# Kernel tuning notes

Hardware: AMD Instinct MI355X
Metric: run time of the kernel (lower is better)

Reference implementation:

```python
import jax, jax.numpy as jnp
import numpy as np
from jax import lax

EPS = 0.1        # entropic regularization
MAX_ITER = 100   # Sinkhorn iteration budget
THRESH = 0.1     # early-stop threshold on err = mean_b sum_i |u - u_prev|
B, N, D = 16, 1024, 64


def setup_inputs() -> dict:
    key = jax.random.key(0)
    k1, k2 = jax.random.split(key)
    x = jax.random.normal(k1, (B, N, D), dtype=jnp.float32)
    y = jax.random.normal(k2, (B, N, D), dtype=jnp.float32)
    return {"x": x, "y": y}


def _lse(A):
    # Faithful to the original (unstabilized) lse: log(sum(exp(A)) + 1e-6)
    return jnp.log(jnp.exp(A).sum(-1) + 1e-6)


def _M(C, u, v):
    # (-C_ij + u_i + v_j) / eps
    return (-C + u[..., :, None] + v[..., None, :]) / EPS


def _cost_matrix(x, y):
    # (avoids materializing the [B, N, N, D] difference tensor; same math for p=2)
    x2 = (x * x).sum(-1)                         # [B, N]
    y2 = (y * y).sum(-1)                         # [B, N]
    xy = jnp.einsum('bid,bjd->bij', x, y)        # [B, N, N]
    return x2[..., :, None] + y2[..., None, :] - 2.0 * xy


def reference(x, y):
    x = jax.nn.softmax(x, axis=-1)
    y = jax.nn.softmax(y, axis=-1)
    C = _cost_matrix(x, y)                       # [B, N, N]
    n = x.shape[-2]
    log_mu = jnp.log(1.0 / n + 1e-8)             # mu = nu = uniform 1/n (scalar broadcast)
    u0 = jnp.zeros((x.shape[0], n), dtype=C.dtype)
    v0 = jnp.zeros_like(u0)

    def cond(carry):
        _, _, i, err = carry
        return jnp.logical_and(i < MAX_ITER, err >= THRESH)

    def body(carry):
        u, v, i, _ = carry
        u1 = u
        u = EPS * (log_mu - _lse(_M(C, u, v))) + u
        v = EPS * (log_mu - _lse(jnp.swapaxes(_M(C, u, v), -2, -1))) + v
        err = jnp.abs(u - u1).sum(-1).mean()
        return (u, v, i + 1, err)

    u, v, _, _ = lax.while_loop(
        cond, body, (u0, v0, jnp.int32(0), jnp.float32(jnp.inf)))

    pi = jnp.exp(_M(C, u, v))                    # transport plan [B, N, N]
    cost = (pi * C).sum((-2, -1))                # [B]
    return cost.mean()                           # reduction='mean'
```

## Files before the change

kernel.cpp:

```cpp
#include <hip/hip_runtime.h>
#include <hip/hip_bf16.h>
#include <math.h>

#define BATCH 16
#define NPTS 1024
#define DIM 64
#define EPSF 0.1f
#define INV_EPS 10.0f
#define MAX_ITER 100
#define THRESHF 0.1f
#define LSTRIDE 72

typedef _Float16 h8 __attribute__((ext_vector_type(8)));
typedef short short8v __attribute__((ext_vector_type(8)));
typedef float float4v __attribute__((ext_vector_type(4)));

#define ATOMIC_ST(p, v) \
  __hip_atomic_store((p), (v), __ATOMIC_RELAXED, __HIP_MEMORY_SCOPE_AGENT)
#define ATOMIC_LD(p) \
  __hip_atomic_load((p), __ATOMIC_RELAXED, __HIP_MEMORY_SCOPE_AGENT)

__device__ inline float waveSum(float x) {
#pragma unroll
  for (int off = 32; off; off >>= 1) x += __shfl_xor(x, off, 64);
  return x;
}
__device__ inline float waveMax(float x) {
#pragma unroll
  for (int off = 32; off; off >>= 1) x = fmaxf(x, __shfl_xor(x, off, 64));
  return x;
}

__global__ __launch_bounds__(512, 1) void sinkhorn_fused(
    const float* __restrict__ x, const float* __restrict__ y,
    __hip_bfloat16* __restrict__ syh,
    float* __restrict__ y2,
    float* __restrict__ colsum,
    float* __restrict__ deltaPub,
    float* __restrict__ errB,
    int* __restrict__ flags,
    float* __restrict__ costPart,
    float* __restrict__ out) {
  __shared__ __attribute__((aligned(16))) short xs[64 * LSTRIDE];
  __shared__ __attribute__((aligned(16))) short ys[2][64 * LSTRIDE];
  __shared__ __attribute__((aligned(16))) short os[2][64 * LSTRIDE];
  __shared__ __attribute__((aligned(16))) float wLDS[NPTS];
  __shared__ __attribute__((aligned(16))) float vLDS[NPTS];
  __shared__ __attribute__((aligned(16))) float colpart[8][NPTS];
  __shared__ float x2L[64];
  __shared__ float derr[8];
  __shared__ float errbL[BATCH];
  const int t = threadIdx.x;
  const int blk = blockIdx.x;
  const int wave = t >> 6, lane = t & 63;
  const int batch = (blk & 7) + 8 * (blk >> 7);
  const int kslot = (blk >> 3) & 15;
  const float log_mu = logf(1.0f / 1024.0f + 1e-8f);

#pragma unroll
  for (int rr = 0; rr < 8; rr++) {
    int rl = wave * 8 + rr;
    int gr = batch * NPTS + kslot * 64 + rl;
    float xv = x[(size_t)gr * DIM + lane];
    float mx = waveMax(xv);
    float ex = expf(xv - mx);
    float sx = waveSum(ex);
    float px = ex / sx;
    __hip_bfloat16 hbx = (__hip_bfloat16)px;
    xs[rl * LSTRIDE + lane] = *(const short*)&hbx;
    float sqx = waveSum(px * px);
    if (lane == 0) x2L[rl] = sqx;
    float yv = y[(size_t)gr * DIM + lane];
    float my = waveMax(yv);
    float ey = expf(yv - my);
    float sy = waveSum(ey);
    float py = ey / sy;
    __hip_bfloat16 hby = (__hip_bfloat16)py;
    unsigned bits = *(const unsigned short*)&hby;
    unsigned nb = __shfl_down(bits, 1);
    if ((lane & 1) == 0)
      ATOMIC_ST((unsigned*)((unsigned short*)syh + (size_t)gr * DIM + lane),
                bits | (nb << 16));
    float sqy = waveSum(py * py);
    if (lane == 0) ATOMIC_ST(&y2[gr], sqy);
  }
  if (t < 192) {
    int buf = t >> 6, j = kslot * 64 + (t & 63);
    ATOMIC_ST(&colsum[((size_t)buf * BATCH + batch) * NPTS + j], 0.f);
  }
  __syncthreads();
  if (t == 0) ATOMIC_ST(&flags[batch * 16 + kslot], 1);
  if (t < 16) {
    while (ATOMIC_LD(&flags[batch * 16 + t]) < 1) {}
  }
  __syncthreads();

  const int m = lane & 15, q = lane >> 4;
  const int g = lane >> 3, sub = lane & 7;
  const int sw = wave & 3, ts = wave >> 2;
  short8v a0 = *(const short8v*)&xs[(sw * 16 + m) * LSTRIDE + q * 8];
  short8v a1 = *(const short8v*)&xs[(sw * 16 + m) * LSTRIDE + 32 + q * 8];
  float xa[4];
#pragma unroll
  for (int reg = 0; reg < 4; reg++) xa[reg] = x2L[sw * 16 + q * 4 + reg];
  h8 ka[8], kb[8];
#pragma unroll
  for (int k = 0; k < 8; k++) {
    {
      int idx = t;
#pragma unroll
      for (int rep = 0; rep < 2; rep++, idx += 512) {
        int r = idx >> 3, c = idx & 7;
        *(short8v*)&ys[r >> 6][(r & 63) * LSTRIDE + c * 8] = *(const short8v*)(
            (const short*)syh + ((size_t)batch * NPTS + 128 * k + r) * DIM + c * 8);
      }
    }
    __syncthreads();
    const int jt = 2 * k + ts;
    float4v accv[4];
#pragma unroll
    for (int tj = 0; tj < 4; tj++) {
      short8v b0 = *(const short8v*)&ys[ts][(tj * 16 + m) * LSTRIDE + q * 8];
      short8v b1 = *(const short8v*)&ys[ts][(tj * 16 + m) * LSTRIDE + 32 + q * 8];
      float4v c = {0.f, 0.f, 0.f, 0.f};
      c = __builtin_amdgcn_mfma_f32_16x16x32_bf16(a0, b0, c, 0, 0, 0);
      c = __builtin_amdgcn_mfma_f32_16x16x32_bf16(a1, b1, c, 0, 0, 0);
      accv[tj] = c;
    }
#pragma unroll
    for (int tj = 0; tj < 4; tj++) {
      float y2v = y2[(size_t)batch * NPTS + jt * 64 + tj * 16 + m];
#pragma unroll
      for (int reg = 0; reg < 4; reg++) {
        float C = xa[reg] + y2v - 2.0f * accv[tj][reg];
        _Float16 kv = (_Float16)expf(-INV_EPS * C);
        os[ts][(sw * 16 + q * 4 + reg) * LSTRIDE + tj * 16 + m] = *(const short*)&kv;
      }
    }
    __syncthreads();
    {
      int e0 = (2 * k) & 7, e1 = (2 * k + 1) & 7;
      if (g == e0 || g == e1) {
        const short* srcp = (g == e0) ? &os[0][0] : &os[1][0];
#pragma unroll
        for (int rr = 0; rr < 8; rr++) {
          h8 v = *(const h8*)&srcp[(wave * 8 + rr) * LSTRIDE + sub * 8];
          if (k < 4) ka[rr] = v; else kb[rr] = v;
        }
      }
    }
    __syncthreads();
  }

  for (int j = t; j < NPTS; j += 512) { vLDS[j] = 0.f; wLDS[j] = 1.f; }
  __syncthreads();

  float u[8], uPrev[8];
#pragma unroll
  for (int r = 0; r < 8; r++) u[r] = 0.f;
  int it = 0;

  while (true) {
#pragma unroll
    for (int r = 0; r < 8; r++) uPrev[r] = u[r];
    const float4* w4 = (const float4*)wLDS;
    float wreg[16];
    *(float4*)&wreg[0]  = w4[2 * lane];
    *(float4*)&wreg[4]  = w4[2 * lane + 1];
    *(float4*)&wreg[8]  = w4[128 + 2 * lane];
    *(float4*)&wreg[12] = w4[128 + 2 * lane + 1];
    float colreg[16];
#pragma unroll
    for (int n = 0; n < 16; n++) colreg[n] = 0.f;
    float delta = 0.f;
#pragma unroll
    for (int rr = 0; rr < 8; rr++) {
      float kf[16];
#pragma unroll
      for (int n = 0; n < 8; n++) {
        kf[n] = (float)ka[rr][n];
        kf[8 + n] = (float)kb[rr][n];
      }
      float dot = 0.f;
#pragma unroll
      for (int n = 0; n < 16; n++) dot = fmaf(kf[n], wreg[n], dot);
      dot = waveSum(dot);
      float uo = u[rr];
      float s = expf(INV_EPS * uo) * dot;
      float un = EPSF * (log_mu - logf(s + 1e-6f)) + uo;
      delta += fabsf(un - uo);
      u[rr] = un;
      float ai = expf(INV_EPS * un);
#pragma unroll
      for (int n = 0; n < 16; n++) colreg[n] = fmaf(kf[n], ai, colreg[n]);
    }
    if (lane == 0) derr[wave] = delta;
    {
      float4* cp = (float4*)&colpart[wave][0];
      cp[2 * lane]       = make_float4(colreg[0], colreg[1], colreg[2], colreg[3]);
      cp[2 * lane + 1]   = make_float4(colreg[4], colreg[5], colreg[6], colreg[7]);
      cp[128 + 2 * lane] = make_float4(colreg[8], colreg[9], colreg[10], colreg[11]);
      cp[128 + 2 * lane + 1] = make_float4(colreg[12], colreg[13], colreg[14], colreg[15]);
    }
    __syncthreads();
    float* cs = colsum + ((size_t)(it % 3) * BATCH + batch) * NPTS;
#pragma unroll
    for (int rep = 0; rep < 2; rep++) {
      int j = t + rep * 512;
      float s = 0.f;
#pragma unroll
      for (int w = 0; w < 8; w++) s += colpart[w][j];
      unsafeAtomicAdd(&cs[j], s);
    }
    if (t == 0) {
      float e = 0.f;
#pragma unroll
      for (int w = 0; w < 8; w++) e += derr[w];
      ATOMIC_ST(&deltaPub[((it & 1) * BATCH + batch) * 16 + kslot], e);
    }
    __syncthreads();
    if (t == 0) ATOMIC_ST(&flags[batch * 16 + kslot], it + 2);
    if (t < 16) {
      while (ATOMIC_LD(&flags[batch * 16 + t]) < it + 2) {}
    }
    __syncthreads();
    float cs0 = ATOMIC_LD(&cs[t]);
    float cs1 = ATOMIC_LD(&cs[t + 512]);
    if (t < 64)
      ATOMIC_ST(&colsum[((size_t)((it + 2) % 3) * BATCH + batch) * NPTS +
                        kslot * 64 + t], 0.f);
    if (kslot == 0 && t == 0) {
      const float* dp = deltaPub + ((it & 1) * BATCH + batch) * 16;
      float e = 0.f;
#pragma unroll
      for (int k = 0; k < 16; k++) e += ATOMIC_LD((float*)&dp[k]);
      ATOMIC_ST(&errB[it * BATCH + batch], e);
    }
    if (it >= 1) {
      if (t < BATCH) {
        float v;
        while ((v = ATOMIC_LD(&errB[(it - 1) * BATCH + t])) < 0.f) {}
        errbL[t] = v;
      }
      __syncthreads();
      float errv = 0.f;
#pragma unroll
      for (int k = 0; k < BATCH; k++) errv += errbL[k];
      if (errv * (1.0f / (float)BATCH) < THRESHF) {
#pragma unroll
        for (int r = 0; r < 8; r++) u[r] = uPrev[r];
        break;
      }
    }
    {
      float vo = vLDS[t];
      float s = expf(INV_EPS * vo) * cs0;
      float vn = EPSF * (log_mu - logf(s + 1e-6f)) + vo;
      vLDS[t] = vn;
      wLDS[t] = expf(INV_EPS * vn);
      float vo1 = vLDS[t + 512];
      float s1 = expf(INV_EPS * vo1) * cs1;
      float vn1 = EPSF * (log_mu - logf(s1 + 1e-6f)) + vo1;
      vLDS[t + 512] = vn1;
      wLDS[t + 512] = expf(INV_EPS * vn1);
    }
    it++;
    if (it >= MAX_ITER) break;
    __syncthreads();
  }

  {
    __syncthreads();
    const float4* w4 = (const float4*)wLDS;
    float wreg[16];
    *(float4*)&wreg[0]  = w4[2 * lane];
    *(float4*)&wreg[4]  = w4[2 * lane + 1];
    *(float4*)&wreg[8]  = w4[128 + 2 * lane];
    *(float4*)&wreg[12] = w4[128 + 2 * lane + 1];
    float csum = 0.f;
#pragma unroll
    for (int rr = 0; rr < 8; rr++) {
      float kf[16];
#pragma unroll
      for (int n = 0; n < 8; n++) {
        kf[n] = (float)ka[rr][n];
        kf[8 + n] = (float)kb[rr][n];
      }
      float ai = expf(INV_EPS * u[rr]);
#pragma unroll
      for (int n = 0; n < 16; n++) {
        if (kf[n] > 0.f)
          csum += ai * wreg[n] * kf[n] * (-EPSF * logf(kf[n]));
      }
    }
    csum = waveSum(csum);
    if (lane == 0) derr[wave] = csum;
    __syncthreads();
    if (t == 0) {
      float cst = 0.f;
#pragma unroll
      for (int w = 0; w < 8; w++) cst += derr[w];
      ATOMIC_ST(&costPart[blk], cst + 1.0f);
    }
    if (blk == 0) {
      if (t < 256) {
        float v;
        while ((v = ATOMIC_LD(&costPart[t])) < 0.5f) {}
        colpart[0][t] = v;
      }
      __syncthreads();
      if (wave == 0) {
        float s = colpart[0][lane] + colpart[0][lane + 64] +
                  colpart[0][lane + 128] + colpart[0][lane + 192];
        s = waveSum(s);
        if (lane == 0) out[0] = (s - 256.0f) * (1.0f / (float)BATCH);
      }
    }
  }
}

extern "C" void kernel_launch(void* const* d_in, const int* in_sizes, int n_in,
                              void* d_out, int out_size, void* d_ws,
                              size_t ws_size, hipStream_t stream) {
  (void)in_sizes; (void)n_in; (void)out_size; (void)ws_size;
  const float* x = (const float*)d_in[0];
  const float* y = (const float*)d_in[1];
  float* out = (float*)d_out;

  char* ws = (char*)d_ws;
  size_t off = 0;
  auto alloc = [&](size_t nbytes) -> void* {
    void* p = (void*)(ws + off);
    off = (off + nbytes + 255) & ~(size_t)255;
    return p;
  };
  __hip_bfloat16* syh = (__hip_bfloat16*)alloc((size_t)BATCH * NPTS * DIM * 2);
  float* y2 = (float*)alloc((size_t)BATCH * NPTS * 4);
  float* colsum = (float*)alloc((size_t)3 * BATCH * NPTS * 4);
  float* deltaPub = (float*)alloc((size_t)2 * BATCH * 16 * 4);
  float* errB = (float*)alloc((size_t)MAX_ITER * BATCH * 4);
  int* flags = (int*)alloc((size_t)BATCH * 16 * 4);
  float* costPart = (float*)alloc(256 * 4);

  void* args[] = {&x, &y, &syh, &y2, &colsum, &deltaPub,
                  &errB, &flags, &costPart, &out};
  hipLaunchCooperativeKernel((void*)sinkhorn_fused, dim3(256), dim3(512), args,
                             0, stream);
}
```

Before: 136.1 us.

## Assign two batches per block to overlap cross-block sync with other batch's work

```diff
diff --git a/kernel.cpp b/kernel.cpp
--- a/kernel.cpp
+++ b/kernel.cpp
@@ -10,6 +10,7 @@
 #define MAX_ITER 100
 #define THRESHF 0.1f
 #define LSTRIDE 72
+#define OSTRIDE 136
 
 typedef _Float16 h8 __attribute__((ext_vector_type(8)));
 typedef short short8v __attribute__((ext_vector_type(8)));
@@ -42,10 +43,11 @@
     float* __restrict__ costPart,
     float* __restrict__ out) {
   __shared__ __attribute__((aligned(16))) short xs[64 * LSTRIDE];
-  __shared__ __attribute__((aligned(16))) short ys[2][64 * LSTRIDE];
-  __shared__ __attribute__((aligned(16))) short os[2][64 * LSTRIDE];
-  __shared__ __attribute__((aligned(16))) float wLDS[NPTS];
-  __shared__ __attribute__((aligned(16))) float vLDS[NPTS];
+  __shared__ __attribute__((aligned(16))) short ysA[128 * LSTRIDE];
+  __shared__ __attribute__((aligned(16))) short ysB[128 * LSTRIDE];
+  __shared__ __attribute__((aligned(16))) short os[2][32 * OSTRIDE];
+  __shared__ __attribute__((aligned(16))) float wV[2][NPTS];
+  __shared__ __attribute__((aligned(16))) float vV[2][NPTS];
   __shared__ __attribute__((aligned(16))) float colpart[8][NPTS];
   __shared__ float x2L[64];
   __shared__ float derr[8];
@@ -53,23 +55,25 @@
   const int t = threadIdx.x;
   const int blk = blockIdx.x;
   const int wave = t >> 6, lane = t & 63;
-  const int batch = (blk & 7) + 8 * (blk >> 7);
-  const int kslot = (blk >> 3) & 15;
+  const int slot = blk >> 3;
+  const int batchA = (blk & 7) * 2;
+  const int batchB = batchA + 1;
   const float log_mu = logf(1.0f / 1024.0f + 1e-8f);
 
 #pragma unroll
   for (int rr = 0; rr < 8; rr++) {
-    int rl = wave * 8 + rr;
-    int gr = batch * NPTS + kslot * 64 + rl;
+    int idx = wave * 8 + rr;
+    int batch = (idx < 32) ? batchA : batchB;
+    int gr = batch * NPTS + slot * 32 + (idx & 31);
     float xv = x[(size_t)gr * DIM + lane];
     float mx = waveMax(xv);
     float ex = expf(xv - mx);
     float sx = waveSum(ex);
     float px = ex / sx;
     __hip_bfloat16 hbx = (__hip_bfloat16)px;
-    xs[rl * LSTRIDE + lane] = *(const short*)&hbx;
+    xs[idx * LSTRIDE + lane] = *(const short*)&hbx;
     float sqx = waveSum(px * px);
-    if (lane == 0) x2L[rl] = sqx;
+    if (lane == 0) x2L[idx] = sqx;
     float yv = y[(size_t)gr * DIM + lane];
     float my = waveMax(yv);
     float ey = expf(yv - my);
@@ -85,157 +89,174 @@
     if (lane == 0) ATOMIC_ST(&y2[gr], sqy);
   }
   if (t < 192) {
-    int buf = t >> 6, j = kslot * 64 + (t & 63);
-    ATOMIC_ST(&colsum[((size_t)buf * BATCH + batch) * NPTS + j], 0.f);
+    int buf = t >> 6, bsel = (t >> 5) & 1, col = slot * 32 + (t & 31);
+    int batch = bsel ? batchB : batchA;
+    ATOMIC_ST(&colsum[((size_t)buf * BATCH + batch) * NPTS + col], 0.f);
   }
   __syncthreads();
-  if (t == 0) ATOMIC_ST(&flags[batch * 16 + kslot], 1);
-  if (t < 16) {
-    while (ATOMIC_LD(&flags[batch * 16 + t]) < 1) {}
+  if (t == 0) ATOMIC_ST(&flags[batchA * 32 + slot], 1);
+  if (t == 1) ATOMIC_ST(&flags[batchB * 32 + slot], 1);
+  if (t < 32) {
+    while (ATOMIC_LD(&flags[batchA * 32 + t]) < 1) {}
+  } else if (t < 64) {
+    while (ATOMIC_LD(&flags[batchB * 32 + (t - 32)]) < 1) {}
   }
   __syncthreads();
 
   const int m = lane & 15, q = lane >> 4;
-  const int g = lane >> 3, sub = lane & 7;
-  const int sw = wave & 3, ts = wave >> 2;
-  short8v a0 = *(const short8v*)&xs[(sw * 16 + m) * LSTRIDE + q * 8];
-  short8v a1 = *(const short8v*)&xs[(sw * 16 + m) * LSTRIDE + 32 + q * 8];
+  const int g16 = lane >> 4, sub16 = lane & 15;
+  const int slabw = wave >> 2;
+  const int ws = wave & 3;
+  const int rt = ws >> 1, cp = ws & 1;
+  short8v a0 = *(const short8v*)&xs[(slabw * 32 + rt * 16 + m) * LSTRIDE + q * 8];
+  short8v a1 = *(const short8v*)&xs[(slabw * 32 + rt * 16 + m) * LSTRIDE + 32 + q * 8];
   float xa[4];
 #pragma unroll
-  for (int reg = 0; reg < 4; reg++) xa[reg] = x2L[sw * 16 + q * 4 + reg];
-  h8 ka[8], kb[8];
+  for (int reg = 0; reg < 4; reg++)
+    xa[reg] = x2L[slabw * 32 + rt * 16 + q * 4 + reg];
+  const int batchW = slabw ? batchB : batchA;
+  h8 ka[2][4], kb[2][4];
 #pragma unroll
   for (int k = 0; k < 8; k++) {
     {
       int idx = t;
 #pragma unroll
-      for (int rep = 0; rep < 2; rep++, idx += 512) {
-        int r = idx >> 3, c = idx & 7;
-        *(short8v*)&ys[r >> 6][(r & 63) * LSTRIDE + c * 8] = *(const short8v*)(
+      for (int rep = 0; rep < 4; rep++, idx += 512) {
+        int bsel = idx >> 10;
+        int r = (idx >> 3) & 127, c = idx & 7;
+        int batch = bsel ? batchB : batchA;
+        short* dst = (bsel ? ysB : ysA) + r * LSTRIDE + c * 8;
+        *(short8v*)dst = *(const short8v*)(
             (const short*)syh + ((size_t)batch * NPTS + 128 * k + r) * DIM + c * 8);
       }
     }
     __syncthreads();
-    const int jt = 2 * k + ts;
+    const short* ys = slabw ? ysB : ysA;
     float4v accv[4];
 #pragma unroll
-    for (int tj = 0; tj < 4; tj++) {
-      short8v b0 = *(const short8v*)&ys[ts][(tj * 16 + m) * LSTRIDE + q * 8];
-      short8v b1 = *(const short8v*)&ys[ts][(tj * 16 + m) * LSTRIDE + 32 + q * 8];
+    for (int i = 0; i < 4; i++) {
+      int ct = cp * 4 + i;
+      short8v b0 = *(const short8v*)&ys[(ct * 16 + m) * LSTRIDE + q * 8];
+      short8v b1 = *(const short8v*)&ys[(ct * 16 + m) * LSTRIDE + 32 + q * 8];
       float4v c = {0.f, 0.f, 0.f, 0.f};
       c = __builtin_amdgcn_mfma_f32_16x16x32_bf16(a0, b0, c, 0, 0, 0);
       c = __builtin_amdgcn_mfma_f32_16x16x32_bf16(a1, b1, c, 0, 0, 0);
-      accv[tj] = c;
-    }
-#pragma unroll
-    for (int tj = 0; tj < 4; tj++) {
-      float y2v = y2[(size_t)batch * NPTS + jt * 64 + tj * 16 + m];
+      accv[i] = c;
+    }
+#pragma unroll
+    for (int i = 0; i < 4; i++) {
+      int ct = cp * 4 + i;
+      float y2v = y2[(size_t)batchW * NPTS + 128 * k + ct * 16 + m];
 #pragma unroll
       for (int reg = 0; reg < 4; reg++) {
-        float C = xa[reg] + y2v - 2.0f * accv[tj][reg];
+        float C = xa[reg] + y2v - 2.0f * accv[i][reg];
         _Float16 kv = (_Float16)expf(-INV_EPS * C);
-        os[ts][(sw * 16 + q * 4 + reg) * LSTRIDE + tj * 16 + m] = *(const short*)&kv;
-      }
-    }
-    __syncthreads();
-    {
-      int e0 = (2 * k) & 7, e1 = (2 * k + 1) & 7;
-      if (g == e0 || g == e1) {
-        const short* srcp = (g == e0) ? &os[0][0] : &os[1][0];
-#pragma unroll
-        for (int rr = 0; rr < 8; rr++) {
-          h8 v = *(const h8*)&srcp[(wave * 8 + rr) * LSTRIDE + sub * 8];
-          if (k < 4) ka[rr] = v; else kb[rr] = v;
+        os[slabw][(rt * 16 + q * 4 + reg) * OSTRIDE + ct * 16 + m] =
+            *(const short*)&kv;
+      }
+    }
+    __syncthreads();
+    if (k < 4) {
+      if (g16 == k) {
+#pragma unroll
+        for (int s = 0; s < 2; s++)
+#pragma unroll
+          for (int rr = 0; rr < 4; rr++)
+            ka[s][rr] = *(const h8*)&os[s][(wave * 4 + rr) * OSTRIDE + sub16 * 8];
+      }
+    } else {
+      if (g16 == k - 4) {
+#pragma unroll
+        for (int s = 0; s < 2; s++)
+#pragma unroll
+          for (int rr = 0; rr < 4; rr++)
+            kb[s][rr] = *(const h8*)&os[s][(wave * 4 + rr) * OSTRIDE + sub16 * 8];
+      }
+    }
+    __syncthreads();
+  }
+
+  for (int j = t; j < NPTS; j += 512) {
+    vV[0][j] = 0.f; wV[0][j] = 1.f;
+    vV[1][j] = 0.f; wV[1][j] = 1.f;
+  }
+  __syncthreads();
+
+  float u[2][4], uPrev[2][4];
+#pragma unroll
+  for (int s = 0; s < 2; s++)
+#pragma unroll
+    for (int r = 0; r < 4; r++) u[s][r] = 0.f;
+  int it = 0;
+
+  while (true) {
+#pragma unroll
+    for (int s = 0; s < 2; s++)
+#pragma unroll
+      for (int r = 0; r < 4; r++) uPrev[s][r] = u[s][r];
+
+#pragma unroll
+    for (int s = 0; s < 2; s++) {
+      const int batch = s ? batchB : batchA;
+      const float4* w4 = (const float4*)wV[s];
+      float wreg[16];
+      *(float4*)&wreg[0]  = w4[2 * lane];
+      *(float4*)&wreg[4]  = w4[2 * lane + 1];
+      *(float4*)&wreg[8]  = w4[128 + 2 * lane];
+      *(float4*)&wreg[12] = w4[128 + 2 * lane + 1];
+      float colreg[16];
+#pragma unroll
+      for (int n = 0; n < 16; n++) colreg[n] = 0.f;
+      float dl = 0.f;
+#pragma unroll
+      for (int rr = 0; rr < 4; rr++) {
+        float kf[16];
+#pragma unroll
+        for (int n = 0; n < 8; n++) {
+          kf[n] = (float)ka[s][rr][n];
+          kf[8 + n] = (float)kb[s][rr][n];
         }
-      }
-    }
-    __syncthreads();
-  }
-
-  for (int j = t; j < NPTS; j += 512) { vLDS[j] = 0.f; wLDS[j] = 1.f; }
-  __syncthreads();
-
-  float u[8], uPrev[8];
-#pragma unroll
-  for (int r = 0; r < 8; r++) u[r] = 0.f;
-  int it = 0;
-
-  while (true) {
-#pragma unroll
-    for (int r = 0; r < 8; r++) uPrev[r] = u[r];
-    const float4* w4 = (const float4*)wLDS;
-    float wreg[16];
-    *(float4*)&wreg[0]  = w4[2 * lane];
-    *(float4*)&wreg[4]  = w4[2 * lane + 1];
-    *(float4*)&wreg[8]  = w4[128 + 2 * lane];
-    *(float4*)&wreg[12] = w4[128 + 2 * lane + 1];
-    float colreg[16];
-#pragma unroll
-    for (int n = 0; n < 16; n++) colreg[n] = 0.f;
-    float delta = 0.f;
-#pragma unroll
-    for (int rr = 0; rr < 8; rr++) {
-      float kf[16];
-#pragma unroll
-      for (int n = 0; n < 8; n++) {
-        kf[n] = (float)ka[rr][n];
-        kf[8 + n] = (float)kb[rr][n];
-      }
-      float dot = 0.f;
-#pragma unroll
-      for (int n = 0; n < 16; n++) dot = fmaf(kf[n], wreg[n], dot);
-      dot = waveSum(dot);
-      float uo = u[rr];
-      float s = expf(INV_EPS * uo) * dot;
-      float un = EPSF * (log_mu - logf(s + 1e-6f)) + uo;
-      delta += fabsf(un - uo);
-      u[rr] = un;
-      float ai = expf(INV_EPS * un);
-#pragma unroll
-      for (int n = 0; n < 16; n++) colreg[n] = fmaf(kf[n], ai, colreg[n]);
-    }
-    if (lane == 0) derr[wave] = delta;
-    {
-      float4* cp = (float4*)&colpart[wave][0];
-      cp[2 * lane]       = make_float4(colreg[0], colreg[1], colreg[2], colreg[3]);
-      cp[2 * lane + 1]   = make_float4(colreg[4], colreg[5], colreg[6], colreg[7]);
-      cp[128 + 2 * lane] = make_float4(colreg[8], colreg[9], colreg[10], colreg[11]);
-      cp[128 + 2 * lane + 1] = make_float4(colreg[12], colreg[13], colreg[14], colreg[15]);
-    }
-    __syncthreads();
-    float* cs = colsum + ((size_t)(it % 3) * BATCH + batch) * NPTS;
-#pragma unroll
-    for (int rep = 0; rep < 2; rep++) {
-      int j = t + rep * 512;
-      float s = 0.f;
-#pragma unroll
-      for (int w = 0; w < 8; w++) s += colpart[w][j];
-      unsafeAtomicAdd(&cs[j], s);
-    }
-    if (t == 0) {
-      float e = 0.f;
-#pragma unroll
-      for (int w = 0; w < 8; w++) e += derr[w];
-      ATOMIC_ST(&deltaPub[((it & 1) * BATCH + batch) * 16 + kslot], e);
-    }
-    __syncthreads();
-    if (t == 0) ATOMIC_ST(&flags[batch * 16 + kslot], it + 2);
-    if (t < 16) {
-      while (ATOMIC_LD(&flags[batch * 16 + t]) < it + 2) {}
-    }
-    __syncthreads();
-    float cs0 = ATOMIC_LD(&cs[t]);
-    float cs1 = ATOMIC_LD(&cs[t + 512]);
-    if (t < 64)
-      ATOMIC_ST(&colsum[((size_t)((it + 2) % 3) * BATCH + batch) * NPTS +
-                        kslot * 64 + t], 0.f);
-    if (kslot == 0 && t == 0) {
-      const float* dp = deltaPub + ((it & 1) * BATCH + batch) * 16;
-      float e = 0.f;
-#pragma unroll
-      for (int k = 0; k < 16; k++) e += ATOMIC_LD((float*)&dp[k]);
-      ATOMIC_ST(&errB[it * BATCH + batch], e);
-    }
+        float dot = 0.f;
+#pragma unroll
+        for (int n = 0; n < 16; n++) dot = fmaf(kf[n], wreg[n], dot);
+        dot = waveSum(dot);
+        float uo = u[s][rr];
+        float sv = expf(INV_EPS * uo) * dot;
+        float un = EPSF * (log_mu - logf(sv + 1e-6f)) + uo;
+        dl += fabsf(un - uo);
+        u[s][rr] = un;
+        float ai = expf(INV_EPS * un);
+#pragma unroll
+        for (int n = 0; n < 16; n++) colreg[n] = fmaf(kf[n], ai, colreg[n]);
+      }
+      if (lane == 0) derr[wave] = dl;
+      {
+        float4* cpv = (float4*)&colpart[wave][0];
+        cpv[2 * lane]       = make_float4(colreg[0], colreg[1], colreg[2], colreg[3]);
+        cpv[2 * lane + 1]   = make_float4(colreg[4], colreg[5], colreg[6], colreg[7]);
+        cpv[128 + 2 * lane] = make_float4(colreg[8], colreg[9], colreg[10], colreg[11]);
+        cpv[128 + 2 * lane + 1] = make_float4(colreg[12], colreg[13], colreg[14], colreg[15]);
+      }
+      __syncthreads();
+      float* cs = colsum + ((size_t)(it % 3) * BATCH + batch) * NPTS;
+#pragma unroll
+      for (int rep = 0; rep < 2; rep++) {
+        int j = t + rep * 512;
+        float sum = 0.f;
+#pragma unroll
+        for (int w = 0; w < 8; w++) sum += colpart[w][j];
+        unsafeAtomicAdd(&cs[j], sum);
+      }
+      if (t == 0) {
+        float e = 0.f;
+#pragma unroll
+        for (int w = 0; w < 8; w++) e += derr[w];
+        ATOMIC_ST(&deltaPub[((it & 1) * BATCH + batch) * 32 + slot], e);
+      }
+      __syncthreads();
+      if (t == 0) ATOMIC_ST(&flags[batch * 32 + slot], it + 2);
+    }
+
     if (it >= 1) {
       if (t < BATCH) {
         float v;
@@ -248,21 +269,43 @@
       for (int k = 0; k < BATCH; k++) errv += errbL[k];
       if (errv * (1.0f / (float)BATCH) < THRESHF) {
 #pragma unroll
-        for (int r = 0; r < 8; r++) u[r] = uPrev[r];
+        for (int s = 0; s < 2; s++)
+#pragma unroll
+          for (int r = 0; r < 4; r++) u[s][r] = uPrev[s][r];
         break;
       }
     }
-    {
-      float vo = vLDS[t];
-      float s = expf(INV_EPS * vo) * cs0;
-      float vn = EPSF * (log_mu - logf(s + 1e-6f)) + vo;
-      vLDS[t] = vn;
-      wLDS[t] = expf(INV_EPS * vn);
-      float vo1 = vLDS[t + 512];
-      float s1 = expf(INV_EPS * vo1) * cs1;
-      float vn1 = EPSF * (log_mu - logf(s1 + 1e-6f)) + vo1;
-      vLDS[t + 512] = vn1;
-      wLDS[t + 512] = expf(INV_EPS * vn1);
+
+#pragma unroll
+    for (int s = 0; s < 2; s++) {
+      const int batch = s ? batchB : batchA;
+      if (t < 32) {
+        while (ATOMIC_LD(&flags[batch * 32 + t]) < it + 2) {}
+      }
+      __syncthreads();
+      float* cs = colsum + ((size_t)(it % 3) * BATCH + batch) * NPTS;
+      float cs0 = ATOMIC_LD(&cs[t]);
+      float cs1 = ATOMIC_LD(&cs[t + 512]);
+      if (t < 32)
+        ATOMIC_ST(&colsum[((size_t)((it + 2) % 3) * BATCH + batch) * NPTS +
+                          slot * 32 + t], 0.f);
+      if (slot == 0 && t == 0) {
+        const float* dp = deltaPub + ((it & 1) * BATCH + batch) * 32;
+        float e = 0.f;
+#pragma unroll
+        for (int k = 0; k < 32; k++) e += ATOMIC_LD((float*)&dp[k]);
+        ATOMIC_ST(&errB[it * BATCH + batch], e);
+      }
+      float vo = vV[s][t];
+      float sv = expf(INV_EPS * vo) * cs0;
+      float vn = EPSF * (log_mu - logf(sv + 1e-6f)) + vo;
+      vV[s][t] = vn;
+      wV[s][t] = expf(INV_EPS * vn);
+      float vo1 = vV[s][t + 512];
+      float sv1 = expf(INV_EPS * vo1) * cs1;
+      float vn1 = EPSF * (log_mu - logf(sv1 + 1e-6f)) + vo1;
+      vV[s][t + 512] = vn1;
+      wV[s][t + 512] = expf(INV_EPS * vn1);
     }
     it++;
     if (it >= MAX_ITER) break;
@@ -271,26 +314,29 @@
 
   {
     __syncthreads();
-    const float4* w4 = (const float4*)wLDS;
-    float wreg[16];
-    *(float4*)&wreg[0]  = w4[2 * lane];
-    *(float4*)&wreg[4]  = w4[2 * lane + 1];
-    *(float4*)&wreg[8]  = w4[128 + 2 * lane];
-    *(float4*)&wreg[12] = w4[128 + 2 * lane + 1];
     float csum = 0.f;
 #pragma unroll
-    for (int rr = 0; rr < 8; rr++) {
-      float kf[16];
-#pragma unroll
-      for (int n = 0; n < 8; n++) {
-        kf[n] = (float)ka[rr][n];
-        kf[8 + n] = (float)kb[rr][n];
-      }
-      float ai = expf(INV_EPS * u[rr]);
-#pragma unroll
-      for (int n = 0; n < 16; n++) {
-        if (kf[n] > 0.f)
-          csum += ai * wreg[n] * kf[n] * (-EPSF * logf(kf[n]));
+    for (int s = 0; s < 2; s++) {
+      const float4* w4 = (const float4*)wV[s];
+      float wreg[16];
+      *(float4*)&wreg[0]  = w4[2 * lane];
+      *(float4*)&wreg[4]  = w4[2 * lane + 1];
+      *(float4*)&wreg[8]  = w4[128 + 2 * lane];
+      *(float4*)&wreg[12] = w4[128 + 2 * lane + 1];
+#pragma unroll
+      for (int rr = 0; rr < 4; rr++) {
+        float kf[16];
+#pragma unroll
+        for (int n = 0; n < 8; n++) {
+          kf[n] = (float)ka[s][rr][n];
+          kf[8 + n] = (float)kb[s][rr][n];
+        }
+        float ai = expf(INV_EPS * u[s][rr]);
+#pragma unroll
+        for (int n = 0; n < 16; n++) {
+          if (kf[n] > 0.f)
+            csum += ai * wreg[n] * kf[n] * (-EPSF * logf(kf[n]));
+        }
       }
     }
     csum = waveSum(csum);
@@ -310,10 +356,10 @@
       }
       __syncthreads();
       if (wave == 0) {
-        float s = colpart[0][lane] + colpart[0][lane + 64] +
-                  colpart[0][lane + 128] + colpart[0][lane + 192];
-        s = waveSum(s);
-        if (lane == 0) out[0] = (s - 256.0f) * (1.0f / (float)BATCH);
+        float sv = colpart[0][lane] + colpart[0][lane + 64] +
+                   colpart[0][lane + 128] + colpart[0][lane + 192];
+        sv = waveSum(sv);
+        if (lane == 0) out[0] = (sv - 256.0f) * (1.0f / (float)BATCH);
       }
     }
   }
@@ -337,9 +383,9 @@
   __hip_bfloat16* syh = (__hip_bfloat16*)alloc((size_t)BATCH * NPTS * DIM * 2);
   float* y2 = (float*)alloc((size_t)BATCH * NPTS * 4);
   float* colsum = (float*)alloc((size_t)3 * BATCH * NPTS * 4);
-  float* deltaPub = (float*)alloc((size_t)2 * BATCH * 16 * 4);
+  float* deltaPub = (float*)alloc((size_t)2 * BATCH * 32 * 4);
   float* errB = (float*)alloc((size_t)MAX_ITER * BATCH * 4);
-  int* flags = (int*)alloc((size_t)BATCH * 16 * 4);
+  int* flags = (int*)alloc((size_t)BATCH * 32 * 4);
   float* costPart = (float*)alloc(256 * 4);
 
   void* args[] = {&x, &y, &syh, &y2, &colsum, &deltaPub,
```

Result: slower. 154.5 us (+13.5%).
